# Optimization experiments

Measured on AMD Instinct MI355X. Metric: run time of the kernel, lower is better.

Reference implementation:

```python
import jax, jax.numpy as jnp
import numpy as np

DIM = 1024
AUX = 3
B, S = 32, 1024
ENC_D = DIM * AUX  # 3072


def setup_inputs() -> dict:
    key = jax.random.key(0)
    ks = jax.random.split(key, 5)
    sc1 = 1.0 / np.sqrt(DIM * (AUX + 1))
    sc3 = 1.0 / np.sqrt(ENC_D)
    return {
        "hidden_state": jax.random.normal(ks[0], (B, DIM), jnp.float32),
        "encoder_outputs": jax.random.normal(ks[1], (B, S, ENC_D), jnp.float32),
        "W1": jax.random.normal(ks[2], (DIM, DIM * (AUX + 1)), jnp.float32) * sc1,
        "b1": jnp.zeros((DIM,), jnp.float32),
        "w2": jax.random.normal(ks[3], (1, DIM), jnp.float32) * (1.0 / np.sqrt(DIM)),
        "W3": jax.random.normal(ks[4], (DIM, ENC_D), jnp.float32) * sc3,
        "b3": jnp.zeros((DIM,), jnp.float32),
    }


def reference(hidden_state, encoder_outputs, W1, b1, w2, W3, b3):
    # hidden_state: (B, dim); encoder_outputs: (B, S, dim*aux)
    Bsz, Slen, _ = encoder_outputs.shape
    h = jnp.broadcast_to(hidden_state[:, None, :], (Bsz, Slen, hidden_state.shape[-1]))
    inputs = jnp.concatenate([encoder_outputs, h], axis=2)  # (B, S, dim*(aux+1))
    # score MLP: tanh(linear1) -> linear2 (no bias)
    hidden = jnp.tanh(jnp.einsum('bsf,df->bsd', inputs, W1) + b1)  # (B, S, dim)
    e = jnp.einsum('bsd,od->bso', hidden, w2)[..., 0]  # (B, S)
    alpha = jax.nn.softmax(e, axis=1)
    context = jnp.einsum('bs,bsf->bf', alpha, encoder_outputs)  # (B, dim*aux)
    return jnp.einsum('bf,df->bd', context, W3) + b3  # (B, dim)
```

## Files before the change

### kernel.cpp

```cpp
#include <hip/hip_runtime.h>
#include <hip/hip_bf16.h>


typedef float          fx4 __attribute__((ext_vector_type(4)));
typedef short          sv8 __attribute__((ext_vector_type(8)));
typedef unsigned short uv8 __attribute__((ext_vector_type(8)));
typedef unsigned short uv4 __attribute__((ext_vector_type(4)));

__device__ __forceinline__ unsigned short f2bf(float x) {
  unsigned u = __float_as_uint(x);
  return (unsigned short)((u + 0x7FFFu + ((u >> 16) & 1u)) >> 16);
}

__device__ __forceinline__ uv8 pack8(fx4 a, fx4 b) {
  uv8 v;
  v[0] = f2bf(a[0]); v[1] = f2bf(a[1]); v[2] = f2bf(a[2]); v[3] = f2bf(a[3]);
  v[4] = f2bf(b[0]); v[5] = f2bf(b[1]); v[6] = f2bf(b[2]); v[7] = f2bf(b[3]);
  return v;
}

__global__ void convw1_kernel(const float* __restrict__ W1, unsigned short* __restrict__ W1a) {
  int id = blockIdx.x * 256 + threadIdx.x;
  int d = id / 768, fi = id - d * 768;
  fx4 v = ((const fx4*)W1)[d * 1024 + fi];
  uv4 r; r[0] = f2bf(v[0]); r[1] = f2bf(v[1]); r[2] = f2bf(v[2]); r[3] = f2bf(v[3]);
  ((uv4*)W1a)[d * 768 + fi] = r;
}

__global__ void hbias_kernel(const float* __restrict__ hs, const float* __restrict__ W1,
                             const float* __restrict__ b1, float* __restrict__ hb) {
  int idx = (blockIdx.x << 2) + (threadIdx.x >> 6);
  int lane = threadIdx.x & 63;
  int b = idx >> 10, d = idx & 1023;
  const fx4* hv = (const fx4*)hs;
  const fx4* wv = (const fx4*)W1;
  float s = 0.f;
#pragma unroll
  for (int i = 0; i < 4; ++i) {
    int k4 = lane + (i << 6);
    fx4 h = hv[(b << 8) + k4];
    fx4 w = wv[d * 1024 + 768 + k4];
    s += h[0] * w[0] + h[1] * w[1] + h[2] * w[2] + h[3] * w[3];
  }
#pragma unroll
  for (int off = 32; off; off >>= 1) s += __shfl_xor(s, off);
  if (lane == 0) hb[idx] = s + b1[d];
}

__global__ __launch_bounds__(256, 2)
void gemm_score(const float* __restrict__ enc,
                const unsigned short* __restrict__ W1a,
                const float* __restrict__ hb,
                const float* __restrict__ w2,
                float* __restrict__ pe) {
  __shared__ __align__(16) unsigned short As[4096];
  __shared__ __align__(16) unsigned short Bs[4096];

  const int t = threadIdx.x;
  const int lane = t & 63, wid = t >> 6;
  const int wm = wid >> 1, wn = wid & 1;

  const int bid = blockIdx.x;
  const int lg = ((bid & 7) << 8) | (bid >> 3);
  const int mt = lg >> 3, nt = lg & 7;
  const int row0 = mt << 7;
  const int col0 = nt << 7;

  const fx4* encv = (const fx4*)enc;
  const uv8* w1v = (const uv8*)W1a;

  fx4 acc[4][4] = {};

  const int c0 = t, c1 = t + 256;
  const int ar0 = c0 >> 2, as0 = c0 & 3;
  const int ar1 = c1 >> 2, as1 = c1 & 3;
  const int st0 = ar0 * 32 + (((as0 ^ (ar0 >> 1)) & 3) << 3);
  const int st1 = ar1 * 32 + (((as1 ^ (ar1 >> 1)) & 3) << 3);
  const int ag0 = (row0 + ar0) * 768 + as0 * 2;
  const int ag1 = (row0 + ar1) * 768 + as1 * 2;
  const int bg0 = (col0 + ar0) * 384 + as0;
  const int bg1 = (col0 + ar1) * 384 + as1;

  fx4 pa0, pa1, pa2, pa3;
  uv8 pb0, pb1;

  const int r15 = lane & 15, q = lane >> 4;
  const int sel = (q ^ (r15 >> 1)) & 3;
  const int offA = (wm * 64 + r15) * 32 + (sel << 3);
  const int offB = (wn * 64 + r15) * 32 + (sel << 3);

  pa0 = encv[ag0]; pa1 = encv[ag0 + 1];
  pa2 = encv[ag1]; pa3 = encv[ag1 + 1];
  pb0 = w1v[bg0];  pb1 = w1v[bg1];
  *(uv8*)&As[st0] = pack8(pa0, pa1);
  *(uv8*)&As[st1] = pack8(pa2, pa3);
  *(uv8*)&Bs[st0] = pb0;
  *(uv8*)&Bs[st1] = pb1;
  __syncthreads();

  for (int kt = 0; kt < 96; ++kt) {
    if (kt < 95) {
      const int k8 = (kt + 1) * 8, k4 = (kt + 1) * 4;
      pa0 = encv[ag0 + k8]; pa1 = encv[ag0 + k8 + 1];
      pa2 = encv[ag1 + k8]; pa3 = encv[ag1 + k8 + 1];
      pb0 = w1v[bg0 + k4];  pb1 = w1v[bg1 + k4];
    }
    sv8 af[4], bf[4];
#pragma unroll
    for (int mi = 0; mi < 4; ++mi) af[mi] = *(const sv8*)&As[offA + mi * 512];
#pragma unroll
    for (int ni = 0; ni < 4; ++ni) bf[ni] = *(const sv8*)&Bs[offB + ni * 512];
#pragma unroll
    for (int mi = 0; mi < 4; ++mi)
#pragma unroll
      for (int ni = 0; ni < 4; ++ni)
        acc[mi][ni] = __builtin_amdgcn_mfma_f32_16x16x32_bf16(af[mi], bf[ni], acc[mi][ni], 0, 0, 0);
    __syncthreads();
    if (kt < 95) {
      *(uv8*)&As[st0] = pack8(pa0, pa1);
      *(uv8*)&As[st1] = pack8(pa2, pa3);
      *(uv8*)&Bs[st0] = pb0;
      *(uv8*)&Bs[st1] = pb1;
    }
    __syncthreads();
  }

  const int b = row0 >> 10;
  float w2v[4], hbv[4];
#pragma unroll
  for (int ni = 0; ni < 4; ++ni) {
    int c = col0 + wn * 64 + ni * 16 + r15;
    w2v[ni] = w2[c];
    hbv[ni] = hb[(b << 10) + c];
  }
#pragma unroll
  for (int mi = 0; mi < 4; ++mi) {
#pragma unroll
    for (int j = 0; j < 4; ++j) {
      float p = 0.f;
#pragma unroll
      for (int ni = 0; ni < 4; ++ni)
        p += tanhf(acc[mi][ni][j] + hbv[ni]) * w2v[ni];
      p += __shfl_xor(p, 1); p += __shfl_xor(p, 2);
      p += __shfl_xor(p, 4); p += __shfl_xor(p, 8);
      if (r15 == 0) {
        int row = row0 + wm * 64 + mi * 16 + (q << 2) + j;
        pe[(row << 4) + (nt << 1) + wn] = p;
      }
    }
  }
}

__global__ void softmax_kernel(const float* __restrict__ pe, float* __restrict__ alpha) {
  int b = blockIdx.x, t = threadIdx.x;
  int lane = t & 63, wid = t >> 6;
  float ev[4];
#pragma unroll
  for (int r = 0; r < 4; ++r) {
    int s = t + r * 256;
    const float* p = pe + ((b << 10) + s) * 16;
    float sum = 0.f;
#pragma unroll
    for (int i = 0; i < 16; ++i) sum += p[i];
    ev[r] = sum;
  }
  float m = fmaxf(fmaxf(ev[0], ev[1]), fmaxf(ev[2], ev[3]));
#pragma unroll
  for (int off = 32; off; off >>= 1) m = fmaxf(m, __shfl_xor(m, off));
  __shared__ float red[8];
  if (lane == 0) red[wid] = m;
  __syncthreads();
  m = fmaxf(fmaxf(red[0], red[1]), fmaxf(red[2], red[3]));
  float p4[4], ls = 0.f;
#pragma unroll
  for (int r = 0; r < 4; ++r) { p4[r] = expf(ev[r] - m); ls += p4[r]; }
#pragma unroll
  for (int off = 32; off; off >>= 1) ls += __shfl_xor(ls, off);
  if (lane == 0) red[4 + wid] = ls;
  __syncthreads();
  float inv = 1.0f / (red[4] + red[5] + red[6] + red[7]);
#pragma unroll
  for (int r = 0; r < 4; ++r) alpha[(b << 10) + t + r * 256] = p4[r] * inv;
}

__global__ void ctxpart_kernel(const float* __restrict__ enc, const float* __restrict__ alpha,
                               float* __restrict__ part) {
  int bid = blockIdx.x, b = bid >> 4, sc = bid & 15;
  int t = threadIdx.x;
  __shared__ float sal[64];
  if (t < 64) sal[t] = alpha[(b << 10) + (sc << 6) + t];
  __syncthreads();
  const fx4* ev = (const fx4*)enc;
  fx4 a0 = {}, a1 = {}, a2 = {};
  int base = ((b << 10) + (sc << 6)) * 768;
  for (int si = 0; si < 64; ++si) {
    float a = sal[si];
    const fx4* rp = ev + base + si * 768;
    a0 += a * rp[t];
    a1 += a * rp[256 + t];
    a2 += a * rp[512 + t];
  }
  fx4* pp = (fx4*)part;
  int pb = ((b << 4) + sc) * 768;
  pp[pb + t] = a0; pp[pb + 256 + t] = a1; pp[pb + 512 + t] = a2;
}

__global__ void ctxreduce_kernel(const float* __restrict__ part, float* __restrict__ ctx) {
  int j = blockIdx.x * 256 + threadIdx.x;
  int b = j / 768, fi = j - b * 768;
  const fx4* pp = (const fx4*)part;
  fx4 s = {};
#pragma unroll
  for (int i = 0; i < 16; ++i) s += pp[((b << 4) + i) * 768 + fi];
  ((fx4*)ctx)[b * 768 + fi] = s;
}

__global__ void final_kernel(const float* __restrict__ ctx, const float* __restrict__ W3,
                             const float* __restrict__ b3, float* __restrict__ out) {
  int idx = (blockIdx.x << 2) + (threadIdx.x >> 6);
  int lane = threadIdx.x & 63;
  int b = idx >> 10, d = idx & 1023;
  const fx4* cv = (const fx4*)ctx;
  const fx4* wv = (const fx4*)W3;
  float s = 0.f;
#pragma unroll
  for (int i = 0; i < 12; ++i) {
    int f4 = lane + (i << 6);
    fx4 c = cv[b * 768 + f4];
    fx4 w = wv[d * 768 + f4];
    s += c[0] * w[0] + c[1] * w[1] + c[2] * w[2] + c[3] * w[3];
  }
#pragma unroll
  for (int off = 32; off; off >>= 1) s += __shfl_xor(s, off);
  if (lane == 0) out[idx] = s + b3[d];
}

extern "C" void kernel_launch(void* const* d_in, const int* in_sizes, int n_in,
                              void* d_out, int out_size, void* d_ws, size_t ws_size,
                              hipStream_t stream) {
  const float* hs  = (const float*)d_in[0];
  const float* enc = (const float*)d_in[1];
  const float* W1  = (const float*)d_in[2];
  const float* b1  = (const float*)d_in[3];
  const float* w2  = (const float*)d_in[4];
  const float* W3  = (const float*)d_in[5];
  const float* b3  = (const float*)d_in[6];
  float* out = (float*)d_out;

  char* ws = (char*)d_ws;
  unsigned short* W1a = (unsigned short*)(ws);
  float* pe    = (float*)(ws + 6291456);
  float* alpha = (float*)(ws + 8388608);
  float* hb    = (float*)(ws + 8519680);
  float* ctx   = (float*)(ws + 8650752);
  float* part  = (float*)(ws + 9043968);

  convw1_kernel<<<3072, 256, 0, stream>>>(W1, W1a);
  hbias_kernel<<<8192, 256, 0, stream>>>(hs, W1, b1, hb);
  gemm_score<<<2048, 256, 0, stream>>>(enc, W1a, hb, w2, pe);
  softmax_kernel<<<32, 256, 0, stream>>>(pe, alpha);
  ctxpart_kernel<<<512, 256, 0, stream>>>(enc, alpha, part);
  ctxreduce_kernel<<<96, 256, 0, stream>>>(part, ctx);
  final_kernel<<<8192, 256, 0, stream>>>(ctx, W3, b3, out);
}
```

Baseline: 482.2 us.

## Enlarge score GEMM tile to 256x128 with double-buffered LDS and direct B loads

```diff
diff --git a/kernel.cpp b/kernel.cpp
--- a/kernel.cpp
+++ b/kernel.cpp
@@ -6,16 +6,22 @@
 typedef short          sv8 __attribute__((ext_vector_type(8)));
 typedef unsigned short uv8 __attribute__((ext_vector_type(8)));
 typedef unsigned short uv4 __attribute__((ext_vector_type(4)));
+typedef unsigned int   ui4 __attribute__((ext_vector_type(4)));
 
 __device__ __forceinline__ unsigned short f2bf(float x) {
   unsigned u = __float_as_uint(x);
   return (unsigned short)((u + 0x7FFFu + ((u >> 16) & 1u)) >> 16);
 }
 
-__device__ __forceinline__ uv8 pack8(fx4 a, fx4 b) {
-  uv8 v;
-  v[0] = f2bf(a[0]); v[1] = f2bf(a[1]); v[2] = f2bf(a[2]); v[3] = f2bf(a[3]);
-  v[4] = f2bf(b[0]); v[5] = f2bf(b[1]); v[6] = f2bf(b[2]); v[7] = f2bf(b[3]);
+__device__ __forceinline__ unsigned cvtpk(float lo, float hi) {
+  unsigned r;
+  asm("v_cvt_pk_bf16_f32 %0, %1, %2" : "=v"(r) : "v"(lo), "v"(hi));
+  return r;
+}
+__device__ __forceinline__ ui4 pack8(fx4 a, fx4 b) {
+  ui4 v;
+  v[0] = cvtpk(a[0], a[1]); v[1] = cvtpk(a[2], a[3]);
+  v[2] = cvtpk(b[0], b[1]); v[3] = cvtpk(b[2], b[3]);
   return v;
 }
 
@@ -53,75 +59,80 @@
                 const float* __restrict__ hb,
                 const float* __restrict__ w2,
                 float* __restrict__ pe) {
-  __shared__ __align__(16) unsigned short As[4096];
-  __shared__ __align__(16) unsigned short Bs[4096];
+  __shared__ __align__(16) unsigned short As[2][8192];
+  __shared__ __align__(16) unsigned short Bs[2][4096];
 
   const int t = threadIdx.x;
   const int lane = t & 63, wid = t >> 6;
   const int wm = wid >> 1, wn = wid & 1;
 
   const int bid = blockIdx.x;
-  const int lg = ((bid & 7) << 8) | (bid >> 3);
+  const int lg = ((bid & 7) << 7) | (bid >> 3);
   const int mt = lg >> 3, nt = lg & 7;
-  const int row0 = mt << 7;
+  const int row0 = mt << 8;
   const int col0 = nt << 7;
 
   const fx4* encv = (const fx4*)enc;
-  const uv8* w1v = (const uv8*)W1a;
-
-  fx4 acc[4][4] = {};
-
-  const int c0 = t, c1 = t + 256;
-  const int ar0 = c0 >> 2, as0 = c0 & 3;
-  const int ar1 = c1 >> 2, as1 = c1 & 3;
-  const int st0 = ar0 * 32 + (((as0 ^ (ar0 >> 1)) & 3) << 3);
-  const int st1 = ar1 * 32 + (((as1 ^ (ar1 >> 1)) & 3) << 3);
-  const int ag0 = (row0 + ar0) * 768 + as0 * 2;
-  const int ag1 = (row0 + ar1) * 768 + as1 * 2;
-  const int bg0 = (col0 + ar0) * 384 + as0;
-  const int bg1 = (col0 + ar1) * 384 + as1;
-
-  fx4 pa0, pa1, pa2, pa3;
-  uv8 pb0, pb1;
+
+  const int arow = t >> 2, asl = t & 3;
+  const int agb = (row0 + arow) * 768 + asl * 2;
+  const int xsl = asl ^ ((t >> 3) & 3);
+  const int ast = arow * 32 + (xsl << 3);
+
+  const int bsw = ((lane & 3) ^ ((lane >> 3) & 3)) << 3;
+  const unsigned short* bsrc0 = W1a + (col0 + wid * 32 + (lane >> 2)) * 3072 + bsw;
+  const unsigned short* bsrc1 = bsrc0 + 16 * 3072;
 
   const int r15 = lane & 15, q = lane >> 4;
   const int sel = (q ^ (r15 >> 1)) & 3;
-  const int offA = (wm * 64 + r15) * 32 + (sel << 3);
+  const int offA = (wm * 128 + r15) * 32 + (sel << 3);
   const int offB = (wn * 64 + r15) * 32 + (sel << 3);
 
-  pa0 = encv[ag0]; pa1 = encv[ag0 + 1];
-  pa2 = encv[ag1]; pa3 = encv[ag1 + 1];
-  pb0 = w1v[bg0];  pb1 = w1v[bg1];
-  *(uv8*)&As[st0] = pack8(pa0, pa1);
-  *(uv8*)&As[st1] = pack8(pa2, pa3);
-  *(uv8*)&Bs[st0] = pb0;
-  *(uv8*)&Bs[st1] = pb1;
+  fx4 acc[8][4] = {};
+  fx4 pa[8];
+
+#define LOAD_A(kt)                                                   \
+  { _Pragma("unroll")                                                \
+    for (int i = 0; i < 4; ++i) {                                    \
+      pa[2*i]   = encv[agb + (kt) * 8 + 49152 * i];                  \
+      pa[2*i+1] = encv[agb + (kt) * 8 + 49152 * i + 1];              \
+    } }
+#define WRITE_A(bq)                                                  \
+  { _Pragma("unroll")                                                \
+    for (int i = 0; i < 4; ++i)                                      \
+      *(ui4*)&As[bq][ast + 2048 * i] = pack8(pa[2*i], pa[2*i+1]); }
+#define LOAD_B(bq, kt)                                               \
+  { __builtin_amdgcn_global_load_lds(                                \
+        (const __attribute__((address_space(1))) void*)(bsrc0 + (kt) * 32), \
+        (__attribute__((address_space(3))) void*)&Bs[bq][wid * 1024],       \
+        16, 0, 0);                                                   \
+    __builtin_amdgcn_global_load_lds(                                \
+        (const __attribute__((address_space(1))) void*)(bsrc1 + (kt) * 32), \
+        (__attribute__((address_space(3))) void*)&Bs[bq][wid * 1024 + 512], \
+        16, 0, 0); }
+
+  LOAD_B(0, 0)
+  LOAD_A(0)
+  WRITE_A(0)
   __syncthreads();
 
   for (int kt = 0; kt < 96; ++kt) {
+    const int p = kt & 1, nx = p ^ 1;
     if (kt < 95) {
-      const int k8 = (kt + 1) * 8, k4 = (kt + 1) * 4;
-      pa0 = encv[ag0 + k8]; pa1 = encv[ag0 + k8 + 1];
-      pa2 = encv[ag1 + k8]; pa3 = encv[ag1 + k8 + 1];
-      pb0 = w1v[bg0 + k4];  pb1 = w1v[bg1 + k4];
+      LOAD_B(nx, kt + 1)
+      LOAD_A(kt + 1)
     }
-    sv8 af[4], bf[4];
-#pragma unroll
-    for (int mi = 0; mi < 4; ++mi) af[mi] = *(const sv8*)&As[offA + mi * 512];
-#pragma unroll
-    for (int ni = 0; ni < 4; ++ni) bf[ni] = *(const sv8*)&Bs[offB + ni * 512];
-#pragma unroll
-    for (int mi = 0; mi < 4; ++mi)
+    sv8 af[8], bfv[4];
+#pragma unroll
+    for (int mi = 0; mi < 8; ++mi) af[mi] = *(const sv8*)&As[p][offA + mi * 512];
+#pragma unroll
+    for (int ni = 0; ni < 4; ++ni) bfv[ni] = *(const sv8*)&Bs[p][offB + ni * 512];
+#pragma unroll
+    for (int mi = 0; mi < 8; ++mi)
 #pragma unroll
       for (int ni = 0; ni < 4; ++ni)
-        acc[mi][ni] = __builtin_amdgcn_mfma_f32_16x16x32_bf16(af[mi], bf[ni], acc[mi][ni], 0, 0, 0);
-    __syncthreads();
-    if (kt < 95) {
-      *(uv8*)&As[st0] = pack8(pa0, pa1);
-      *(uv8*)&As[st1] = pack8(pa2, pa3);
-      *(uv8*)&Bs[st0] = pb0;
-      *(uv8*)&Bs[st1] = pb1;
-    }
+        acc[mi][ni] = __builtin_amdgcn_mfma_f32_16x16x32_bf16(af[mi], bfv[ni], acc[mi][ni], 0, 0, 0);
+    if (kt < 95) WRITE_A(nx)
     __syncthreads();
   }
 
@@ -134,21 +145,24 @@
     hbv[ni] = hb[(b << 10) + c];
   }
 #pragma unroll
-  for (int mi = 0; mi < 4; ++mi) {
+  for (int mi = 0; mi < 8; ++mi) {
 #pragma unroll
     for (int j = 0; j < 4; ++j) {
-      float p = 0.f;
+      float pz = 0.f;
 #pragma unroll
       for (int ni = 0; ni < 4; ++ni)
-        p += tanhf(acc[mi][ni][j] + hbv[ni]) * w2v[ni];
-      p += __shfl_xor(p, 1); p += __shfl_xor(p, 2);
-      p += __shfl_xor(p, 4); p += __shfl_xor(p, 8);
+        pz += tanhf(acc[mi][ni][j] + hbv[ni]) * w2v[ni];
+      pz += __shfl_xor(pz, 1); pz += __shfl_xor(pz, 2);
+      pz += __shfl_xor(pz, 4); pz += __shfl_xor(pz, 8);
       if (r15 == 0) {
-        int row = row0 + wm * 64 + mi * 16 + (q << 2) + j;
-        pe[(row << 4) + (nt << 1) + wn] = p;
+        int row = row0 + wm * 128 + mi * 16 + (q << 2) + j;
+        pe[(row << 4) + (nt << 1) + wn] = pz;
       }
     }
   }
+#undef LOAD_A
+#undef WRITE_A
+#undef LOAD_B
 }
 
 __global__ void softmax_kernel(const float* __restrict__ pe, float* __restrict__ alpha) {
@@ -257,7 +271,7 @@
 
   convw1_kernel<<<3072, 256, 0, stream>>>(W1, W1a);
   hbias_kernel<<<8192, 256, 0, stream>>>(hs, W1, b1, hb);
-  gemm_score<<<2048, 256, 0, stream>>>(enc, W1a, hb, w2, pe);
+  gemm_score<<<1024, 256, 0, stream>>>(enc, W1a, hb, w2, pe);
   softmax_kernel<<<32, 256, 0, stream>>>(pe, alpha);
   ctxpart_kernel<<<512, 256, 0, stream>>>(enc, alpha, part);
   ctxreduce_kernel<<<96, 256, 0, stream>>>(part, ctx);
```

New measurement: 610.2 us. 1.27x slower.
